# Optimization experiments

Hardware: AMD Instinct MI355X
Metric: run time of the kernel (lower is better)

The kernel has to match this reference:

```python
import jax, jax.numpy as jnp
import numpy as np


def _l2norm(x, axis):
    return x / jnp.maximum(jnp.linalg.norm(x, axis=axis, keepdims=True), 1e-12)


def setup_inputs() -> dict:
    key = jax.random.key(0)
    ks = jax.random.split(key, 16)
    N, D, F, TI, HD = 1000, 100, 100, 512, 128
    # binary doc-word membership masks, ~50 words per document
    masks = (jax.random.uniform(ks[0], (D, N)) < 0.05).astype(jnp.float32)
    # sparse symmetric normalized word-graph adjacency
    a = (jax.random.uniform(ks[1], (N, N)) < 0.01).astype(jnp.float32)
    adj = jnp.maximum(a, a.T) + jnp.eye(N, dtype=jnp.float32)
    dinv = 1.0 / jnp.sqrt(adj.sum(axis=1))
    train_adj = adj * dinv[:, None] * dinv[None, :]
    bows_vec = jax.random.normal(ks[2], (N, F), dtype=jnp.float32) * 0.1
    image_features = jax.random.normal(ks[3], (D, TI), dtype=jnp.float32)

    def sc(i, sh):
        return jax.random.normal(ks[i], sh, dtype=jnp.float32) * np.float32(1.0 / np.sqrt(sh[0]))

    return {
        'epoch': 3, 'epochs': 10,
        'train_adj': train_adj, 'masks': masks, 'bows_vec': bows_vec,
        'image_features': image_features,
        'W_g1': sc(4, (F, F)), 'W_g2': sc(5, (F, F)),
        'W_h1': sc(6, (F, F)), 'b_h1': jnp.zeros(F, jnp.float32),
        'W_h2': sc(7, (F, F)), 'b_h2': jnp.zeros(F, jnp.float32),
        'W_mu2': sc(8, (F, 1)), 'b_mu2': jnp.zeros(1, jnp.float32),
        'W_eta2': sc(9, (F, 1)), 'b_eta2': jnp.zeros(1, jnp.float32),
        'W_gamma2': sc(10, (F, 1)), 'b_gamma2': jnp.zeros(1, jnp.float32),
        'w_m': sc(11, (F, 1)), 'W_beta': sc(12, (F, 1)),
        'W_m1': sc(13, (TI, HD)), 'b_m1': jnp.zeros(HD, jnp.float32),
        'W_m2': sc(14, (HD, 1)), 'b_m2': jnp.zeros(1, jnp.float32),
    }


def reference(epoch, epochs, train_adj, masks, bows_vec, image_features,
              W_g1, W_g2, W_h1, b_h1, W_h2, b_h2,
              W_mu2, b_mu2, W_eta2, b_eta2, W_gamma2, b_gamma2,
              w_m, W_beta, W_m1, b_m1, W_m2, b_m2):
    N = train_adj.shape[0]
    # --- GcnNet: 2-layer GCN over word graph; doc embedding = masked mean pool ---
    H1 = jax.nn.relu(train_adj @ (bows_vec @ W_g1))        # [N,100]
    H = train_adj @ (H1 @ W_g2)                            # [N,100]
    cnt = masks.sum(axis=1, keepdims=True)                 # [D,1]
    H_p = (masks @ H) / jnp.maximum(cnt, 1.0)              # [D,100]

    H_eli = jax.nn.relu(jax.nn.relu(H @ W_h1 + b_h1) @ W_h2 + b_h2)
    H_eli_norm = _l2norm(H_eli, axis=1)                    # [N,100]

    mu = jax.nn.relu(H_p @ W_mu2 + b_mu2)                  # [D,1]
    # dropout disabled (eval mode)
    eta = jax.nn.relu(H_p @ W_eta2 + b_eta2)               # [D,1]
    gamma = jax.nn.relu(H_p @ W_gamma2 + b_gamma2)         # [D,1]

    sparsity = (epoch / epochs) * 0.3                      # python float (static)
    flat = w_m.reshape(-1)
    j = int(round(sparsity * flat.shape[0]))
    order = jnp.argsort(flat)                              # ascending; drop lowest j
    binary = jnp.zeros_like(flat).at[order[j:]].set(1.0)
    mask_ste = flat + jax.lax.stop_gradient(binary - flat) # forward==binary
    w_pruned = mask_ste.reshape(-1, 1) * W_beta            # [100,1]
    beta_ = _l2norm((H @ w_pruned)[:, 0], axis=0)          # [N]
    beta = masks @ beta_[:, None]                          # [D,1]

    Z_ = jax.nn.relu(H_eli_norm @ H_eli_norm.T)            # [N,N]

    # per-doc sum over distinct word pairs of h_i . h_j ; ||h||=1 so
    # sum_{a<b} h_a.h_b = (||sum_a h_a||^2 - k)/2 with k = #words in doc
    s = masks @ H_eli_norm                                 # [D,100]
    k = masks.sum(axis=1)                                  # [D]
    Z = jax.nn.relu(0.5 * (jnp.sum(s * s, axis=1) - k))[:, None]  # [D,1]

    # Z_event: per-doc [N,N] with entries at local positions p,q < k_i (p!=q)
    # (original indexes Z_ with LOCAL sorted positions 0..k_i-1; kept faithful)
    pos = jnp.arange(N)
    valid = (pos[None, :] < k[:, None]).astype(jnp.float32)       # [D,N]
    E = jnp.exp(-jnp.square(2.0 - 2.0 * Z_)) * (1.0 - jnp.eye(N)) # [N,N]
    Z_event = E[None, :, :] * valid[:, :, None] * valid[:, None, :]  # [D,N,N]

    lambda_texts = jax.nn.sigmoid(mu + beta + eta * jnp.exp(-gamma * Z))
    h_img = jax.nn.relu(image_features @ W_m1 + b_m1)
    lambda_imgs = h_img @ W_m2 + b_m2                      # MLP(512,128,1)
    lambda_total = jax.nn.sigmoid(lambda_texts + lambda_imgs)
    return (lambda_total, Z_, beta_, gamma, eta, Z_event, H)
```

## Files before the change

### kernel.cpp

```cpp
#include <hip/hip_runtime.h>
#include <hip/hip_bf16.h>

typedef __hip_bfloat16 bf;

#define NN   1000
#define DD   100
#define FF   100
#define TIF  512
#define HDD  128
#define EB   256
#define ACAP 96
#define MCAP 192

#define O_LAM 0
#define O_Z   100
#define O_B3  1000100
#define O_GAM 1001100
#define O_ETA 1001200
#define O_ZE  1001300
#define O_H   101001300

__device__ __forceinline__ float ldf(const void* p, int i, int F32){
  return F32 ? ((const float*)p)[i] : __bfloat162float(((const __hip_bfloat16*)p)[i]);
}

__device__ __forceinline__ float blk_red(float v, volatile float* red, int tid){
#pragma unroll
  for (int o=32;o>0;o>>=1) v += __shfl_down(v,o,64);
  if ((tid&63)==0) red[tid>>6]=v;
  __syncthreads();
  float r = red[0]+red[1];
  __syncthreads();
  return r;
}

__global__ void k_sniff(const unsigned short* __restrict__ p, int* flag){
  int lane = threadIdx.x;
  int cnt = 0;
  for (int i=lane; i<8192; i+=64){
    unsigned e = (p[i]>>7)&0xFFu;
    cnt += (e>=0xE0u) ? 1 : 0;
  }
#pragma unroll
  for (int o=32;o>0;o>>=1) cnt += __shfl_down(cnt,o,64);
  if (lane==0) flag[0] = (cnt>16) ? 1 : 0;
}

__global__ void k_zero(uint4* __restrict__ p16, long n16){
  long i = (long)blockIdx.x*blockDim.x + threadIdx.x;
  long st = (long)gridDim.x*blockDim.x;
  uint4 z; z.x=z.y=z.z=z.w=0u;
  for (; i<n16; i+=st) p16[i]=z;
}

__global__ void k_build(const void* __restrict__ A, const void* __restrict__ masks,
                        const void* __restrict__ wm, const void* __restrict__ Wbeta,
                        const int* epoch, const int* epochs, const int* flag,
                        int* a_idx, float* a_val, int* a_nnz,
                        int* m_idx, int* m_cnt, float* wpr, float* sumsq){
  int b = blockIdx.x; int lane = threadIdx.x;
  int F32 = flag[0];
  if (b < NN){
    int i=b, nn=0;
    for (int base=0;base<NN;base+=64){
      int c=base+lane; float v=0.f;
      if (c<NN) v=ldf(A, i*NN+c, F32);
      unsigned long long m=__ballot(v!=0.f);
      if (v!=0.f){
        int pos=nn+__popcll(m&((1ull<<lane)-1ull));
        if (pos<ACAP){ a_idx[i*ACAP+pos]=c; a_val[i*ACAP+pos]=v; }
      }
      nn+=__popcll(m);
    }
    if (lane==0) a_nnz[i]=min(nn,ACAP);
  } else if (b < NN+DD){
    int d=b-NN, nn=0;
    for (int base=0;base<NN;base+=64){
      int c=base+lane; float v=0.f;
      if (c<NN) v=ldf(masks, d*NN+c, F32);
      unsigned long long m=__ballot(v!=0.f);
      if (v!=0.f){
        int pos=nn+__popcll(m&((1ull<<lane)-1ull));
        if (pos<MCAP) m_idx[d*MCAP+pos]=c;
      }
      nn+=__popcll(m);
    }
    if (lane==0) m_cnt[d]=min(nn,MCAP);
  } else {
    __shared__ float w[FF];
    for (int t=lane;t<FF;t+=64) w[t]=ldf(wm, t, F32);
    __syncthreads();
    float sp = 0.3f*(float)epoch[0]/(float)epochs[0];
    int j=(int)lroundf(sp*(float)FF);
    for (int t=lane;t<FF;t+=64){
      float v=w[t]; int r=0;
      for (int u=0;u<FF;u++){ float vu=w[u]; r += ((vu<v)||(vu==v && u<t)) ? 1 : 0; }
      wpr[t] = (r>=j)? ldf(Wbeta, t, F32) : 0.f;
    }
    if (lane==0) sumsq[0]=0.f;
  }
}

template<bool WSRC>
__global__ void k_mm100(const void* __restrict__ Asrc, const void* __restrict__ W,
                        const int* flag, float* __restrict__ C){
  int row=blockIdx.x, tx=threadIdx.x;
  int F32 = flag[0];
  __shared__ float ar[FF];
  if (WSRC){ const float* Af=(const float*)Asrc; for(int t=tx;t<FF;t+=128) ar[t]=Af[row*FF+t]; }
  else     { for(int t=tx;t<FF;t+=128) ar[t]=ldf(Asrc, row*FF+t, F32); }
  __syncthreads();
  if (tx<FF){
    float a=0.f;
#pragma unroll 4
    for (int c=0;c<FF;c++) a=fmaf(ar[c], ldf(W, c*FF+tx, F32), a);
    C[row*FF+tx]=a;
  }
}

__global__ void k_spmm(const float* __restrict__ B, const int* __restrict__ a_idx,
                       const float* __restrict__ a_val, const int* __restrict__ a_nnz,
                       float* __restrict__ C, float* __restrict__ outb, int relu){
  int row=blockIdx.x, tx=threadIdx.x;
  __shared__ int sidx[ACAP]; __shared__ float sval[ACAP];
  int nn=a_nnz[row];
  for (int t=tx;t<nn;t+=128){ sidx[t]=a_idx[row*ACAP+t]; sval[t]=a_val[row*ACAP+t]; }
  __syncthreads();
  if (tx<FF){
    float a=0.f;
    for (int m=0;m<nn;m++) a=fmaf(sval[m], B[sidx[m]*FF+tx], a);
    if (relu) a=fmaxf(a,0.f);
    C[row*FF+tx]=a;
    if (outb) outb[row*FF+tx]=a;
  }
}

__global__ void k_rowchain(const float* __restrict__ Hh,
                           const void* __restrict__ Wh1, const void* __restrict__ bh1,
                           const void* __restrict__ Wh2, const void* __restrict__ bh2,
                           const float* __restrict__ wpr, const int* flag,
                           float* __restrict__ Hn, float* __restrict__ HnT,
                           float* __restrict__ hw, float* sumsq){
  int i=blockIdx.x, tx=threadIdx.x;
  int F32 = flag[0];
  __shared__ float hr[FF], t1[FF];
  __shared__ float red[2];
  for (int t=tx;t<FF;t+=128) hr[t]=Hh[i*FF+t];
  __syncthreads();
  if (tx<FF){
    float a=ldf(bh1, tx, F32);
#pragma unroll 4
    for (int c=0;c<FF;c++) a=fmaf(hr[c], ldf(Wh1, c*FF+tx, F32), a);
    t1[tx]=fmaxf(a,0.f);
  }
  __syncthreads();
  float hel=0.f;
  if (tx<FF){
    float s=ldf(bh2, tx, F32);
#pragma unroll 4
    for (int c=0;c<FF;c++) s=fmaf(t1[c], ldf(Wh2, c*FF+tx, F32), s);
    hel=fmaxf(s,0.f);
  }
  float phw = (tx<FF)? hr[tx]*wpr[tx] : 0.f;
  float rs2 = blk_red(hel*hel, red, tx);
  float rhw = blk_red(phw, red, tx);
  float rinv = 1.f/fmaxf(sqrtf(rs2), 1e-12f);
  if (tx<FF){ float v=hel*rinv; Hn[i*FF+tx]=v; HnT[tx*NN+i]=v; }
  if (tx==0){ hw[i]=rhw; atomicAdd(sumsq, rhw*rhw); }
}

__global__ void k_doc(const float* __restrict__ Hh, const float* __restrict__ Hn,
                      const float* __restrict__ hw, const float* __restrict__ sumsq,
                      const int* __restrict__ m_idx, const int* __restrict__ m_cnt,
                      const void* Wmu, const void* bmu, const void* Weta, const void* beta_b,
                      const void* Wgam, const void* bgam, const int* flag,
                      float* v_lt, int* v_k, float* __restrict__ out){
  int d=blockIdx.x, tx=threadIdx.x;
  int F32 = flag[0];
  __shared__ int sidx[MCAP]; __shared__ float red[2];
  int cnt=m_cnt[d];
  for (int t=tx;t<cnt;t+=128) sidx[t]=m_idx[d*MCAP+t];
  __syncthreads();
  float accH=0.f, accS=0.f;
  if (tx<FF) for (int m=0;m<cnt;m++){ int n=sidx[m]; accH+=Hh[n*FF+tx]; accS+=Hn[n*FF+tx]; }
  float Hp = accH/fmaxf((float)cnt,1.f);
  float pmu = (tx<FF)? Hp*ldf(Wmu, tx, F32)  : 0.f;
  float peta= (tx<FF)? Hp*ldf(Weta, tx, F32) : 0.f;
  float pgam= (tx<FF)? Hp*ldf(Wgam, tx, F32) : 0.f;
  float phw=0.f;
  for (int m=tx;m<cnt;m+=128) phw+=hw[sidx[m]];
  float rmu =blk_red(pmu,red,tx);
  float reta=blk_red(peta,red,tx);
  float rgam=blk_red(pgam,red,tx);
  float rs2 =blk_red(accS*accS,red,tx);
  float rhw =blk_red(phw,red,tx);
  if (tx==0){
    float mu =fmaxf(rmu +ldf(bmu,0,F32),   0.f);
    float eta=fmaxf(reta+ldf(beta_b,0,F32),0.f);
    float gam=fmaxf(rgam+ldf(bgam,0,F32),  0.f);
    float Zd =fmaxf(0.5f*(rs2-(float)cnt), 0.f);
    float beta=rhw/fmaxf(sqrtf(sumsq[0]),1e-12f);
    float lt=1.f/(1.f+expf(-(mu+beta+eta*expf(-gam*Zd))));
    v_lt[d]=lt; v_k[d]=cnt;
    out[O_GAM+d]=gam;
    out[O_ETA+d]=eta;
  }
}

__global__ __launch_bounds__(256) void k_z(const float* __restrict__ HnT,
                                           float* __restrict__ outZ, float* __restrict__ Eblk){
  int bi=blockIdx.x*64, bj=blockIdx.y*64;
  __shared__ float At[FF*68], Bt[FF*68];
  int tid=threadIdx.x;
  for (int t=tid;t<FF*64;t+=256){
    int k=t>>6, ii=t&63;
    int gi=bi+ii, gj=bj+ii;
    At[k*68+ii] = (gi<NN)? HnT[k*NN+gi] : 0.f;
    Bt[k*68+ii] = (gj<NN)? HnT[k*NN+gj] : 0.f;
  }
  __syncthreads();
  int tx=tid&15, ty=tid>>4;
  float acc[4][4]={};
  for (int k=0;k<FF;k++){
    float4 av=*(float4*)&At[k*68+4*ty];
    float4 bv=*(float4*)&Bt[k*68+4*tx];
    float aa[4]={av.x,av.y,av.z,av.w};
    float bb[4]={bv.x,bv.y,bv.z,bv.w};
#pragma unroll
    for (int q=0;q<4;q++)
#pragma unroll
      for (int r=0;r<4;r++) acc[q][r]=fmaf(aa[q],bb[r],acc[q][r]);
  }
#pragma unroll
  for (int q=0;q<4;q++){
    int gi=bi+4*ty+q; if (gi>=NN) continue;
    float z[4];
#pragma unroll
    for (int r=0;r<4;r++) z[r]=fmaxf(acc[q][r],0.f);
    int gj0=bj+4*tx;
    if (gj0+3<NN){
      float4 zz; zz.x=z[0]; zz.y=z[1]; zz.z=z[2]; zz.w=z[3];
      *(float4*)&outZ[(size_t)gi*NN+gj0]=zz;
    } else {
      for (int r=0;r<4;r++) if (gj0+r<NN) outZ[(size_t)gi*NN+gj0+r]=z[r];
    }
    if (gi<EB && gj0<EB){
#pragma unroll
      for (int r=0;r<4;r++){
        int gj=gj0+r;
        float t2=2.f-2.f*z[r];
        Eblk[gi*EB+gj]=(gi==gj)?0.f:expf(-t2*t2);
      }
    }
  }
}

__global__ void k_img(const void* __restrict__ img, const void* __restrict__ Wm1,
                      const void* __restrict__ bm1, const void* __restrict__ Wm2,
                      const void* __restrict__ bm2, const int* flag,
                      const float* __restrict__ v_lt, const float* __restrict__ hw,
                      const float* __restrict__ sumsq, float* __restrict__ out){
  int b=blockIdx.x, tx=threadIdx.x;
  int F32 = flag[0];
  if (b<DD){
    __shared__ float ir[TIF]; __shared__ float red[2];
    for (int t=tx;t<TIF;t+=128) ir[t]=ldf(img, b*TIF+t, F32);
    __syncthreads();
    float a=ldf(bm1, tx, F32);
#pragma unroll 4
    for (int t=0;t<TIF;t++) a=fmaf(ir[t], ldf(Wm1, t*HDD+tx, F32), a);
    a=fmaxf(a,0.f);
    float r=blk_red(a*ldf(Wm2, tx, F32), red, tx);
    if (tx==0){
      float limg=r+ldf(bm2,0,F32);
      out[O_LAM+b]=1.f/(1.f+expf(-(v_lt[b]+limg)));
    }
  } else {
    int i=(b-DD)*128+tx;
    if (i<NN){
      float rinv=1.f/fmaxf(sqrtf(sumsq[0]),1e-12f);
      out[O_B3+i]=hw[i]*rinv;
    }
  }
}

__global__ void k_fill(const float* __restrict__ Eblk, const int* __restrict__ v_k,
                       float* __restrict__ outZE){
  int d=blockIdx.x; int k=v_k[d]; if (k>EB) k=EB;
  int kk=k*k;
  for (int idx=threadIdx.x; idx<kk; idx+=256){
    int i=idx/k, j=idx-i*k;
    float e=(i==j)?0.f:Eblk[i*EB+j];
    outZE[(size_t)d*1000000 + (size_t)i*1000 + j]=e;
  }
}

extern "C" void kernel_launch(void* const* d_in, const int* in_sizes, int n_in,
                              void* d_out, int out_size, void* d_ws, size_t ws_size,
                              hipStream_t stream) {
  const int* epoch  = (const int*)d_in[0];
  const int* epochs = (const int*)d_in[1];
  const void* A     = d_in[2];
  const void* masks = d_in[3];
  const void* X     = d_in[4];
  const void* img   = d_in[5];
  const void* Wg1   = d_in[6];
  const void* Wg2   = d_in[7];
  const void* Wh1   = d_in[8];
  const void* bh1   = d_in[9];
  const void* Wh2   = d_in[10];
  const void* bh2   = d_in[11];
  const void* Wmu   = d_in[12];
  const void* bmu   = d_in[13];
  const void* Weta  = d_in[14];
  const void* beta_b= d_in[15];
  const void* Wgam  = d_in[16];
  const void* bgam  = d_in[17];
  const void* wm    = d_in[18];
  const void* Wbeta = d_in[19];
  const void* Wm1   = d_in[20];
  const void* bm1   = d_in[21];
  const void* Wm2   = d_in[22];
  const void* bm2   = d_in[23];
  float* out = (float*)d_out;

  float* ws   = (float*)d_ws;
  float* XW   = ws;
  float* H1   = XW  + 100000;
  float* H1W  = H1  + 100000;
  float* Hh   = H1W + 100000;
  float* Hn   = Hh  + 100000;
  float* HnT  = Hn  + 100000;
  float* Eblk = HnT + 100000;
  float* a_val= Eblk+ 65536;
  int* a_idx  = (int*)(a_val + 96000);
  int* a_nnz  = a_idx + 96000;
  int* m_idx  = a_nnz + 1000;
  int* m_cnt  = m_idx + 19200;
  float* wpr  = (float*)(m_cnt + 100);
  float* hw   = wpr + 100;
  float* sumsq= hw + 1000;
  float* v_lt = sumsq + 4;
  int* v_k    = (int*)(v_lt + 100);
  int* flag   = v_k + 100;

  hipLaunchKernelGGL(k_sniff, dim3(1), dim3(64), 0, stream,
                     (const unsigned short*)X, flag);
  {
    uint4* p16 = (uint4*)((char*)d_out + (size_t)O_ZE*4);
    long n16 = (long)(400000000LL/16);
    hipLaunchKernelGGL(k_zero, dim3(4096), dim3(256), 0, stream, p16, n16);
  }
  hipLaunchKernelGGL(k_build, dim3(NN+DD+1), dim3(64), 0, stream,
                     A, masks, wm, Wbeta, epoch, epochs, flag,
                     a_idx, a_val, a_nnz, m_idx, m_cnt, wpr, sumsq);
  hipLaunchKernelGGL((k_mm100<false>), dim3(NN), dim3(128), 0, stream, X, Wg1, flag, XW);
  hipLaunchKernelGGL(k_spmm, dim3(NN), dim3(128), 0, stream, XW, a_idx, a_val, a_nnz, H1, (float*)nullptr, 1);
  hipLaunchKernelGGL((k_mm100<true>), dim3(NN), dim3(128), 0, stream, (const void*)H1, Wg2, flag, H1W);
  hipLaunchKernelGGL(k_spmm, dim3(NN), dim3(128), 0, stream, H1W, a_idx, a_val, a_nnz, Hh, out + O_H, 0);
  hipLaunchKernelGGL(k_rowchain, dim3(NN), dim3(128), 0, stream,
                     Hh, Wh1, bh1, Wh2, bh2, wpr, flag, Hn, HnT, hw, sumsq);
  hipLaunchKernelGGL(k_doc, dim3(DD), dim3(128), 0, stream,
                     Hh, Hn, hw, sumsq, m_idx, m_cnt,
                     Wmu, bmu, Weta, beta_b, Wgam, bgam, flag, v_lt, v_k, out);
  hipLaunchKernelGGL(k_z, dim3(16,16), dim3(256), 0, stream, HnT, out + O_Z, Eblk);
  hipLaunchKernelGGL(k_img, dim3(DD+8), dim3(128), 0, stream,
                     img, Wm1, bm1, Wm2, bm2, flag, v_lt, hw, sumsq, out);
  hipLaunchKernelGGL(k_fill, dim3(DD), dim3(256), 0, stream, Eblk, v_k, out + O_ZE);
}
```

Before: 705.7 us.

## Distribute output zero-fill across compute kernels and fold sniff/img into others

Removes the standalone zeroing kernel for the 400MB Z_event output and splits the memset into spans handled by extra blocks appended to each compute kernel. The small pipeline kernels then run alongside bandwidth-bound zeroing. The dtype sniff is inlined per block, the image MLP moves into k_build, and the beta output moves into k_doc, which removes two launches. Zeroing stays ordered before k_fill because all kernels share one stream. The trade-off is more complex kernels and possibly uneven zero spans across kernels.

```diff
diff --git a/kernel.cpp b/kernel.cpp
--- a/kernel.cpp
+++ b/kernel.cpp
@@ -20,6 +20,8 @@
 #define O_ZE  1001300
 #define O_H   101001300
 
+#define ZTOT 25000000L
+
 __device__ __forceinline__ float ldf(const void* p, int i, int F32){
   return F32 ? ((const float*)p)[i] : __bfloat162float(((const __hip_bfloat16*)p)[i]);
 }
@@ -34,32 +36,42 @@
   return r;
 }
 
-__global__ void k_sniff(const unsigned short* __restrict__ p, int* flag){
-  int lane = threadIdx.x;
-  int cnt = 0;
-  for (int i=lane; i<8192; i+=64){
-    unsigned e = (p[i]>>7)&0xFFu;
-    cnt += (e>=0xE0u) ? 1 : 0;
-  }
-#pragma unroll
-  for (int o=32;o>0;o>>=1) cnt += __shfl_down(cnt,o,64);
-  if (lane==0) flag[0] = (cnt>16) ? 1 : 0;
-}
-
-__global__ void k_zero(uint4* __restrict__ p16, long n16){
-  long i = (long)blockIdx.x*blockDim.x + threadIdx.x;
-  long st = (long)gridDim.x*blockDim.x;
+__device__ __forceinline__ int sniffF32(const unsigned short* __restrict__ p, int tid){
+  int lane = tid & 63;
+  const ushort4* q = (const ushort4*)p;
+  ushort4 a = q[lane*2], b = q[lane*2+1];
+  int c = 0;
+  c += (((a.x>>7)&0xFF)>=0xE0); c += (((a.y>>7)&0xFF)>=0xE0);
+  c += (((a.z>>7)&0xFF)>=0xE0); c += (((a.w>>7)&0xFF)>=0xE0);
+  c += (((b.x>>7)&0xFF)>=0xE0); c += (((b.y>>7)&0xFF)>=0xE0);
+  c += (((b.z>>7)&0xFF)>=0xE0); c += (((b.w>>7)&0xFF)>=0xE0);
+#pragma unroll
+  for (int o=32;o>0;o>>=1) c += __shfl_xor(c,o,64);
+  return c > 8;
+}
+
+__device__ __forceinline__ void zero_span(uint4* __restrict__ zb, long off, long cnt,
+                                          int zi, int nzb, int tid, int bdim){
+  long per = (cnt + nzb - 1)/nzb;
+  long s = (long)zi*per; if (s>cnt) s=cnt;
+  long e = s+per; if (e>cnt) e=cnt;
   uint4 z; z.x=z.y=z.z=z.w=0u;
-  for (; i<n16; i+=st) p16[i]=z;
+  for (long i=off+s+tid; i<off+e; i+=bdim) zb[i]=z;
 }
 
 __global__ void k_build(const void* __restrict__ A, const void* __restrict__ masks,
                         const void* __restrict__ wm, const void* __restrict__ Wbeta,
-                        const int* epoch, const int* epochs, const int* flag,
+                        const void* __restrict__ img, const void* __restrict__ Wm1,
+                        const void* __restrict__ bm1, const void* __restrict__ Wm2,
+                        const void* __restrict__ bm2,
+                        const unsigned short* __restrict__ Xu16,
+                        const int* epoch, const int* epochs,
                         int* a_idx, float* a_val, int* a_nnz,
-                        int* m_idx, int* m_cnt, float* wpr, float* sumsq){
+                        int* m_idx, int* m_cnt, float* wpr, float* sumsq,
+                        float* limg, int* flag, uint4* __restrict__ zb){
   int b = blockIdx.x; int lane = threadIdx.x;
-  int F32 = flag[0];
+  if (b >= NN+DD+1+DD){ zero_span(zb, 0L, 5500000L, b-(NN+DD+1+DD), 1024, lane, 64); return; }
+  int F32 = sniffF32(Xu16, lane);
   if (b < NN){
     int i=b, nn=0;
     for (int base=0;base<NN;base+=64){
@@ -86,7 +98,7 @@
       nn+=__popcll(m);
     }
     if (lane==0) m_cnt[d]=min(nn,MCAP);
-  } else {
+  } else if (b == NN+DD){
     __shared__ float w[FF];
     for (int t=lane;t<FF;t+=64) w[t]=ldf(wm, t, F32);
     __syncthreads();
@@ -97,14 +109,31 @@
       for (int u=0;u<FF;u++){ float vu=w[u]; r += ((vu<v)||(vu==v && u<t)) ? 1 : 0; }
       wpr[t] = (r>=j)? ldf(Wbeta, t, F32) : 0.f;
     }
-    if (lane==0) sumsq[0]=0.f;
+    if (lane==0){ sumsq[0]=0.f; flag[0]=F32; }
+  } else {
+    int d = b - (NN+DD+1);
+    __shared__ float ir[TIF];
+    for (int t=lane;t<TIF;t+=64) ir[t]=ldf(img, d*TIF+t, F32);
+    __syncthreads();
+    float acc=0.f;
+    for (int h=lane; h<HDD; h+=64){
+      float a=ldf(bm1, h, F32);
+#pragma unroll 4
+      for (int t=0;t<TIF;t++) a=fmaf(ir[t], ldf(Wm1, t*HDD+h, F32), a);
+      acc = fmaf(fmaxf(a,0.f), ldf(Wm2, h, F32), acc);
+    }
+#pragma unroll
+    for (int o=32;o>0;o>>=1) acc += __shfl_down(acc,o,64);
+    if (lane==0) limg[d]=acc+ldf(bm2,0,F32);
   }
 }
 
 template<bool WSRC>
 __global__ void k_mm100(const void* __restrict__ Asrc, const void* __restrict__ W,
-                        const int* flag, float* __restrict__ C){
+                        const int* flag, float* __restrict__ C,
+                        uint4* __restrict__ zb, long zoff){
   int row=blockIdx.x, tx=threadIdx.x;
+  if (row >= NN){ zero_span(zb, zoff, 2000000L, row-NN, 512, tx, 128); return; }
   int F32 = flag[0];
   __shared__ float ar[FF];
   if (WSRC){ const float* Af=(const float*)Asrc; for(int t=tx;t<FF;t+=128) ar[t]=Af[row*FF+t]; }
@@ -120,8 +149,10 @@
 
 __global__ void k_spmm(const float* __restrict__ B, const int* __restrict__ a_idx,
                        const float* __restrict__ a_val, const int* __restrict__ a_nnz,
-                       float* __restrict__ C, float* __restrict__ outb, int relu){
+                       float* __restrict__ C, float* __restrict__ outb, int relu,
+                       uint4* __restrict__ zb, long zoff){
   int row=blockIdx.x, tx=threadIdx.x;
+  if (row >= NN){ zero_span(zb, zoff, 2000000L, row-NN, 512, tx, 128); return; }
   __shared__ int sidx[ACAP]; __shared__ float sval[ACAP];
   int nn=a_nnz[row];
   for (int t=tx;t<nn;t+=128){ sidx[t]=a_idx[row*ACAP+t]; sval[t]=a_val[row*ACAP+t]; }
@@ -140,8 +171,10 @@
                            const void* __restrict__ Wh2, const void* __restrict__ bh2,
                            const float* __restrict__ wpr, const int* flag,
                            float* __restrict__ Hn, float* __restrict__ HnT,
-                           float* __restrict__ hw, float* sumsq){
+                           float* __restrict__ hw, float* sumsq,
+                           uint4* __restrict__ zb){
   int i=blockIdx.x, tx=threadIdx.x;
+  if (i >= NN){ zero_span(zb, 13500000L, 4000000L, i-NN, 1024, tx, 128); return; }
   int F32 = flag[0];
   __shared__ float hr[FF], t1[FF];
   __shared__ float red[2];
@@ -174,8 +207,18 @@
                       const int* __restrict__ m_idx, const int* __restrict__ m_cnt,
                       const void* Wmu, const void* bmu, const void* Weta, const void* beta_b,
                       const void* Wgam, const void* bgam, const int* flag,
-                      float* v_lt, int* v_k, float* __restrict__ out){
+                      const float* __restrict__ limg,
+                      int* v_k, float* __restrict__ out, uint4* __restrict__ zb){
   int d=blockIdx.x, tx=threadIdx.x;
+  if (d >= DD+8){ zero_span(zb, 17500000L, 1500000L, d-(DD+8), 384, tx, 128); return; }
+  if (d >= DD){
+    int i=(d-DD)*128+tx;
+    if (i<NN){
+      float rinv=1.f/fmaxf(sqrtf(sumsq[0]),1e-12f);
+      out[O_B3+i]=hw[i]*rinv;
+    }
+    return;
+  }
   int F32 = flag[0];
   __shared__ int sidx[MCAP]; __shared__ float red[2];
   int cnt=m_cnt[d];
@@ -201,17 +244,21 @@
     float Zd =fmaxf(0.5f*(rs2-(float)cnt), 0.f);
     float beta=rhw/fmaxf(sqrtf(sumsq[0]),1e-12f);
     float lt=1.f/(1.f+expf(-(mu+beta+eta*expf(-gam*Zd))));
-    v_lt[d]=lt; v_k[d]=cnt;
+    v_k[d]=cnt;
+    out[O_LAM+d]=1.f/(1.f+expf(-(lt+limg[d])));
     out[O_GAM+d]=gam;
     out[O_ETA+d]=eta;
   }
 }
 
 __global__ __launch_bounds__(256) void k_z(const float* __restrict__ HnT,
-                                           float* __restrict__ outZ, float* __restrict__ Eblk){
-  int bi=blockIdx.x*64, bj=blockIdx.y*64;
+                                           float* __restrict__ outZ, float* __restrict__ Eblk,
+                                           uint4* __restrict__ zb){
+  int b = blockIdx.x;
+  int tid=threadIdx.x;
+  if (b >= 256){ zero_span(zb, 19000000L, 6000000L, b-256, 1024, tid, 256); return; }
+  int bi=(b&15)*64, bj=(b>>4)*64;
   __shared__ float At[FF*68], Bt[FF*68];
-  int tid=threadIdx.x;
   for (int t=tid;t<FF*64;t+=256){
     int k=t>>6, ii=t&63;
     int gi=bi+ii, gj=bj+ii;
@@ -251,35 +298,6 @@
         float t2=2.f-2.f*z[r];
         Eblk[gi*EB+gj]=(gi==gj)?0.f:expf(-t2*t2);
       }
-    }
-  }
-}
-
-__global__ void k_img(const void* __restrict__ img, const void* __restrict__ Wm1,
-                      const void* __restrict__ bm1, const void* __restrict__ Wm2,
-                      const void* __restrict__ bm2, const int* flag,
-                      const float* __restrict__ v_lt, const float* __restrict__ hw,
-                      const float* __restrict__ sumsq, float* __restrict__ out){
-  int b=blockIdx.x, tx=threadIdx.x;
-  int F32 = flag[0];
-  if (b<DD){
-    __shared__ float ir[TIF]; __shared__ float red[2];
-    for (int t=tx;t<TIF;t+=128) ir[t]=ldf(img, b*TIF+t, F32);
-    __syncthreads();
-    float a=ldf(bm1, tx, F32);
-#pragma unroll 4
-    for (int t=0;t<TIF;t++) a=fmaf(ir[t], ldf(Wm1, t*HDD+tx, F32), a);
-    a=fmaxf(a,0.f);
-    float r=blk_red(a*ldf(Wm2, tx, F32), red, tx);
-    if (tx==0){
-      float limg=r+ldf(bm2,0,F32);
-      out[O_LAM+b]=1.f/(1.f+expf(-(v_lt[b]+limg)));
-    }
-  } else {
-    int i=(b-DD)*128+tx;
-    if (i<NN){
-      float rinv=1.f/fmaxf(sqrtf(sumsq[0]),1e-12f);
-      out[O_B3+i]=hw[i]*rinv;
     }
   }
 }
@@ -340,31 +358,25 @@
   float* wpr  = (float*)(m_cnt + 100);
   float* hw   = wpr + 100;
   float* sumsq= hw + 1000;
-  float* v_lt = sumsq + 4;
-  int* v_k    = (int*)(v_lt + 100);
-  int* flag   = v_k + 100;
-
-  hipLaunchKernelGGL(k_sniff, dim3(1), dim3(64), 0, stream,
-                     (const unsigned short*)X, flag);
-  {
-    uint4* p16 = (uint4*)((char*)d_out + (size_t)O_ZE*4);
-    long n16 = (long)(400000000LL/16);
-    hipLaunchKernelGGL(k_zero, dim3(4096), dim3(256), 0, stream, p16, n16);
-  }
-  hipLaunchKernelGGL(k_build, dim3(NN+DD+1), dim3(64), 0, stream,
-                     A, masks, wm, Wbeta, epoch, epochs, flag,
-                     a_idx, a_val, a_nnz, m_idx, m_cnt, wpr, sumsq);
-  hipLaunchKernelGGL((k_mm100<false>), dim3(NN), dim3(128), 0, stream, X, Wg1, flag, XW);
-  hipLaunchKernelGGL(k_spmm, dim3(NN), dim3(128), 0, stream, XW, a_idx, a_val, a_nnz, H1, (float*)nullptr, 1);
-  hipLaunchKernelGGL((k_mm100<true>), dim3(NN), dim3(128), 0, stream, (const void*)H1, Wg2, flag, H1W);
-  hipLaunchKernelGGL(k_spmm, dim3(NN), dim3(128), 0, stream, H1W, a_idx, a_val, a_nnz, Hh, out + O_H, 0);
-  hipLaunchKernelGGL(k_rowchain, dim3(NN), dim3(128), 0, stream,
-                     Hh, Wh1, bh1, Wh2, bh2, wpr, flag, Hn, HnT, hw, sumsq);
-  hipLaunchKernelGGL(k_doc, dim3(DD), dim3(128), 0, stream,
+  int* v_k    = (int*)(sumsq + 4);
+  int* flag   = v_k + 104;
+  float* limg = (float*)(flag + 4);
+
+  uint4* zb = (uint4*)((char*)d_out + (size_t)O_ZE*4);
+
+  hipLaunchKernelGGL(k_build, dim3(NN+DD+1+DD+1024), dim3(64), 0, stream,
+                     A, masks, wm, Wbeta, img, Wm1, bm1, Wm2, bm2,
+                     (const unsigned short*)X, epoch, epochs,
+                     a_idx, a_val, a_nnz, m_idx, m_cnt, wpr, sumsq, limg, flag, zb);
+  hipLaunchKernelGGL((k_mm100<false>), dim3(NN+512), dim3(128), 0, stream, X, Wg1, flag, XW, zb, 5500000L);
+  hipLaunchKernelGGL(k_spmm, dim3(NN+512), dim3(128), 0, stream, XW, a_idx, a_val, a_nnz, H1, (float*)nullptr, 1, zb, 7500000L);
+  hipLaunchKernelGGL((k_mm100<true>), dim3(NN+512), dim3(128), 0, stream, (const void*)H1, Wg2, flag, H1W, zb, 9500000L);
+  hipLaunchKernelGGL(k_spmm, dim3(NN+512), dim3(128), 0, stream, H1W, a_idx, a_val, a_nnz, Hh, out + O_H, 0, zb, 11500000L);
+  hipLaunchKernelGGL(k_rowchain, dim3(NN+1024), dim3(128), 0, stream,
+                     Hh, Wh1, bh1, Wh2, bh2, wpr, flag, Hn, HnT, hw, sumsq, zb);
+  hipLaunchKernelGGL(k_doc, dim3(DD+8+384), dim3(128), 0, stream,
                      Hh, Hn, hw, sumsq, m_idx, m_cnt,
-                     Wmu, bmu, Weta, beta_b, Wgam, bgam, flag, v_lt, v_k, out);
-  hipLaunchKernelGGL(k_z, dim3(16,16), dim3(256), 0, stream, HnT, out + O_Z, Eblk);
-  hipLaunchKernelGGL(k_img, dim3(DD+8), dim3(128), 0, stream,
-                     img, Wm1, bm1, Wm2, bm2, flag, v_lt, hw, sumsq, out);
+                     Wmu, bmu, Weta, beta_b, Wgam, bgam, flag, limg, v_k, out, zb);
+  hipLaunchKernelGGL(k_z, dim3(256+1024), dim3(256), 0, stream, HnT, out + O_Z, Eblk, zb);
   hipLaunchKernelGGL(k_fill, dim3(DD), dim3(256), 0, stream, Eblk, v_k, out + O_ZE);
 }
```

Result: no change. 694.6 us (-1.6%).
